# Optimization experiments

Hardware: AMD Instinct MI355X
Metric: run time of the kernel (lower is better)

Reference implementation:

```python
import jax, jax.numpy as jnp
import numpy as np

N = 50000
E = 1600000
IN_DIM = 256
HID = 64
OUT = 16
NEG_SLOPE = 0.01


def setup_inputs() -> dict:
    key = jax.random.key(0)
    ks = jax.random.split(key, 6)
    local_features = jax.random.normal(ks[0], (N, IN_DIM), dtype=jnp.float32)
    edge_index = jax.random.randint(ks[1], (2, E), 0, N, dtype=jnp.int32)
    W0 = jax.random.normal(ks[2], (IN_DIM, HID), dtype=jnp.float32) * 0.05
    a0 = jax.random.normal(ks[3], (2 * HID, 1), dtype=jnp.float32) * 0.05
    W1 = jax.random.normal(ks[4], (HID, OUT), dtype=jnp.float32) * 0.05
    a1 = jax.random.normal(ks[5], (2 * OUT, 1), dtype=jnp.float32) * 0.05
    return {"local_features": local_features, "edge_index": edge_index,
            "W0": W0, "a0": a0, "W1": W1, "a1": a1}


def _segment_softmax(scores, seg, num_segments):
    # softmax over edges sharing the same row (destination) id
    smax = jax.ops.segment_max(scores, seg, num_segments=num_segments)
    ex = jnp.exp(scores - smax[seg])
    ssum = jax.ops.segment_sum(ex, seg, num_segments=num_segments)
    return ex / ssum[seg]


def _gat_layer(H, row, col, W, a, apply_elu):
    d = W.shape[1]
    Hw = H @ W                                   # [N, d]
    # score_e = leaky_relu([Hw[row] || Hw[col]] @ a) = leaky_relu(pr[row] + pc[col])
    pr = Hw @ a[:d, 0]                           # [N]
    pc = Hw @ a[d:, 0]                           # [N]
    s = pr[row] + pc[col]                        # [E]
    s = jnp.where(s >= 0, s, NEG_SLOPE * s)      # leaky_relu
    att = _segment_softmax(s, row, Hw.shape[0])  # per-row sparse softmax (dim=1)
    # out[row] = sum_e att_e * Hw[col_e]
    out = jax.ops.segment_sum(att[:, None] * Hw[col], row, num_segments=Hw.shape[0])
    if apply_elu:
        out = jnp.where(out > 0, out, jnp.expm1(out))  # elu
    return out


def reference(local_features, edge_index, W0, a0, W1, a1):
    row = edge_index[0]
    col = edge_index[1]
    H = _gat_layer(local_features, row, col, W0, a0, apply_elu=True)
    H = _gat_layer(H, row, col, W1, a1, apply_elu=False)
    return jax.nn.log_softmax(H, axis=1)
```

## Files before the change

### kernel.cpp

```cpp
#include <hip/hip_runtime.h>
#include <hip/hip_bf16.h>
#include <math.h>

#define NN 50000
#define NE 1600000
#define BSH 9
#define BCK 98
#define BCAP 20480

typedef __attribute__((ext_vector_type(8))) short bf16x8;
typedef __attribute__((ext_vector_type(4))) float f32x4;

__device__ __forceinline__ short f2bf(float f) {
    return (short)((__float_as_uint(f) + 0x8000u) >> 16);
}
__device__ __forceinline__ float bf2f(ushort u) {
    return __uint_as_float(((unsigned)u) << 16);
}
__device__ __forceinline__ float lo16(unsigned u) { return __uint_as_float(u << 16); }
__device__ __forceinline__ float hi16(unsigned u) { return __uint_as_float(u & 0xffff0000u); }
__device__ __forceinline__ unsigned enc_f(float f) {
    unsigned u = __float_as_uint(f);
    return (u & 0x80000000u) ? ~u : (u | 0x80000000u);
}
__device__ __forceinline__ float dec_f(unsigned e) {
    return (e & 0x80000000u) ? __uint_as_float(e & 0x7FFFFFFFu)
                             : __uint_as_float(~e);
}

__global__ void initcur_kernel(int* __restrict__ gcursor, unsigned* __restrict__ maxes) {
    int b = threadIdx.x;
    if (b < BCK) gcursor[b] = b * BCAP;
    if (b < 2) maxes[b] = 0u;
}

__global__ void __launch_bounds__(1024) binA_kernel(
        const int* __restrict__ row, const int* __restrict__ col,
        int* __restrict__ gcursor, unsigned* __restrict__ staging) {
    __shared__ unsigned lds_stage[8192];
    __shared__ unsigned lds_addr[8192];
    __shared__ int lds_cnt[128];
    __shared__ int lds_off[128];
    __shared__ int wg_goff[128];
    __shared__ int wtot[2];
    int t = threadIdx.x;
    int lane = t & 63;
    int w = t >> 6;

    for (int cb = blockIdx.x * 8192; cb < NE; cb += gridDim.x * 8192) {
        int cnt_edges = NE - cb; if (cnt_edges > 8192) cnt_edges = 8192;
        if (t < 128) lds_cnt[t] = 0;
        __syncthreads();
        int myb[8]; int mylo[8]; unsigned mypk[8];
        #pragma unroll
        for (int i = 0; i < 8; ++i) {
            int idx = i * 1024 + t;
            myb[i] = -1;
            if (idx < cnt_edges) {
                int e = cb + idx;
                int r = row[e], c = col[e];
                int b = r >> BSH;
                myb[i] = b;
                mypk[i] = ((unsigned)(r & 511) << 16) | (unsigned)c;
                mylo[i] = atomicAdd(&lds_cnt[b], 1);
            }
        }
        __syncthreads();
        int v = (t < 128) ? lds_cnt[t] : 0;
        int x = v;
        #pragma unroll
        for (int off = 1; off < 64; off <<= 1) {
            int y = __shfl_up(x, off);
            if (lane >= off) x += y;
        }
        if (t < 128 && lane == 63) wtot[w] = x;
        __syncthreads();
        int add = (w == 1) ? wtot[0] : 0;
        if (t < 128) lds_off[t] = x - v + add;
        if (t < BCK) {
            int cc = lds_cnt[t];
            wg_goff[t] = cc ? atomicAdd(&gcursor[t], cc) : 0;
        }
        __syncthreads();
        #pragma unroll
        for (int i = 0; i < 8; ++i) if (myb[i] >= 0) {
            int p = lds_off[myb[i]] + mylo[i];
            lds_stage[p] = mypk[i];
            lds_addr[p] = (unsigned)(wg_goff[myb[i]] + mylo[i]);
        }
        __syncthreads();
        for (int i = t; i < cnt_edges; i += 1024)
            staging[lds_addr[i]] = lds_stage[i];
        __syncthreads();
    }
}

__global__ void bucketscan_kernel(const int* __restrict__ gcursor,
                                  int* __restrict__ bbase,
                                  int* __restrict__ rowptr) {
    __shared__ int wt0;
    int t = threadIdx.x;
    int lane = t & 63;
    int w = t >> 6;
    int v = (t < BCK) ? (gcursor[t] - t * BCAP) : 0;
    int x = v;
    #pragma unroll
    for (int off = 1; off < 64; off <<= 1) {
        int y = __shfl_up(x, off);
        if (lane >= off) x += y;
    }
    if (w == 0 && lane == 63) wt0 = x;
    __syncthreads();
    int excl = x - v + ((w == 1) ? wt0 : 0);
    if (t < BCK) bbase[t] = excl;
    if (t == BCK - 1) { bbase[BCK] = excl + v; rowptr[NN] = excl + v; }
}

__global__ void __launch_bounds__(1024) binB_kernel(
        const int* __restrict__ bbase,
        const unsigned* __restrict__ staging,
        int* __restrict__ rowptr,
        ushort* __restrict__ colperm) {
    __shared__ int cur[512];
    __shared__ int lexcl[512];
    __shared__ int wls[8];
    __shared__ ushort lds_col[BCAP];
    int b = blockIdx.x;
    int t = threadIdx.x;
    int lane = t & 63;
    int w = t >> 6;
    int rbase = b << BSH;
    int nrows = NN - rbase; if (nrows > 512) nrows = 512;
    int gbase = bbase[b];
    int cnt = bbase[b + 1] - gbase;
    if (cnt > BCAP) cnt = BCAP;
    const unsigned* sb = staging + (size_t)b * BCAP;

    if (t < 512) cur[t] = 0;
    __syncthreads();
    for (int i = t; i < cnt; i += 1024)
        atomicAdd(&cur[sb[i] >> 16], 1);
    __syncthreads();
    int v = 0, x = 0;
    if (t < 512) {
        v = cur[t];
        x = v;
        #pragma unroll
        for (int off = 1; off < 64; off <<= 1) {
            int y = __shfl_up(x, off);
            if (lane >= off) x += y;
        }
        if (lane == 63) wls[w] = x;
    }
    __syncthreads();
    if (t < 8) {
        int s = wls[t];
        #pragma unroll
        for (int off = 1; off < 8; off <<= 1) {
            int y = __shfl_up(s, off, 8);
            if ((t & 7) >= off) s += y;
        }
        wls[t] = s;
    }
    __syncthreads();
    if (t < 512) {
        int e = x - v + ((w > 0) ? wls[w - 1] : 0);
        lexcl[t] = e;
        if (t < nrows) rowptr[rbase + t] = gbase + e;
    }
    __syncthreads();
    if (t < 512) cur[t] = lexcl[t];
    __syncthreads();
    for (int i = t; i < cnt; i += 1024) {
        unsigned e = sb[i];
        int pos = atomicAdd(&cur[e >> 16], 1);
        lds_col[pos] = (ushort)(e & 0xFFFFu);
    }
    __syncthreads();
    for (int i = t; i < cnt; i += 1024)
        colperm[gbase + i] = lds_col[i];
}

__global__ void pcmax_kernel(const float* __restrict__ pc, unsigned* __restrict__ out) {
    int i = blockIdx.x * 256 + threadIdx.x;
    float v = (i < NN) ? pc[i] : -1e30f;
    #pragma unroll
    for (int off = 32; off; off >>= 1) v = fmaxf(v, __shfl_xor(v, off));
    if ((threadIdx.x & 63) == 0) atomicMax(out, enc_f(v));
}

__global__ void prep_kernel(const float* __restrict__ W, ushort* __restrict__ WTg) {
    int i = blockIdx.x * 256 + threadIdx.x;
    if (i >= 64 * 256) return;
    int n = i >> 8, k = i & 255;
    WTg[n * 264 + k] = (ushort)f2bf(W[k * 64 + n]);
}

__global__ void __launch_bounds__(256) gemm0_kernel(
        const float* __restrict__ X,
        const ushort* __restrict__ WTg,
        const float* __restrict__ a,
        __hip_bfloat16* __restrict__ Hwb,
        float* __restrict__ pr,
        float* __restrict__ pc) {
    __shared__ ushort Wt[64 * 264];
    int tid = threadIdx.x;
    {
        const uint* src = (const uint*)WTg;
        uint* dst = (uint*)Wt;
        for (int i = tid; i < 64 * 132; i += 256) dst[i] = src[i];
    }
    __syncthreads();
    int lane = tid & 63, wid = tid >> 6;
    int c = lane & 15, quad = lane >> 4;
    const ushort* wtp[4];
#pragma unroll
    for (int g = 0; g < 4; ++g) wtp[g] = &Wt[(g * 16 + c) * 264 + quad * 8];
    float aA[4], aB[4];
#pragma unroll
    for (int g = 0; g < 4; ++g) { aA[g] = a[g * 16 + c]; aB[g] = a[64 + g * 16 + c]; }

    int row0 = blockIdx.x * 128 + wid * 16;

#pragma unroll
    for (int tt = 0; tt < 2; ++tt) {
        int rt = row0 + tt * 64;
        int arow = rt + c; if (arow >= NN) arow = NN - 1;
        const float* xbase = X + (size_t)arow * 256 + quad * 8;
        f32x4 acc[4];
#pragma unroll
        for (int g = 0; g < 4; ++g) acc[g] = (f32x4){0.f, 0.f, 0.f, 0.f};

#pragma unroll
        for (int k0 = 0; k0 < 256; k0 += 32) {
            float4 xa = *(const float4*)(xbase + k0);
            float4 xb = *(const float4*)(xbase + k0 + 4);
            bf16x8 af;
            af[0] = f2bf(xa.x); af[1] = f2bf(xa.y); af[2] = f2bf(xa.z); af[3] = f2bf(xa.w);
            af[4] = f2bf(xb.x); af[5] = f2bf(xb.y); af[6] = f2bf(xb.z); af[7] = f2bf(xb.w);
#pragma unroll
            for (int g = 0; g < 4; ++g) {
                bf16x8 bg = *(const bf16x8*)(wtp[g] + k0);
                acc[g] = __builtin_amdgcn_mfma_f32_16x16x32_bf16(af, bg, acc[g], 0, 0, 0);
            }
        }

#pragma unroll
        for (int r = 0; r < 4; ++r) {
            int row = rt + quad * 4 + r;
            float v0 = acc[0][r], v1 = acc[1][r], v2 = acc[2][r], v3 = acc[3][r];
            if (row < NN) {
                __hip_bfloat16* hp = Hwb + (size_t)row * 64 + c;
                hp[0]  = __float2bfloat16(v0);
                hp[16] = __float2bfloat16(v1);
                hp[32] = __float2bfloat16(v2);
                hp[48] = __float2bfloat16(v3);
            }
            float pv = v0 * aA[0] + v1 * aA[1] + v2 * aA[2] + v3 * aA[3];
            float qv = v0 * aB[0] + v1 * aB[1] + v2 * aB[2] + v3 * aB[3];
#pragma unroll
            for (int off = 8; off; off >>= 1) {
                pv += __shfl_xor(pv, off);
                qv += __shfl_xor(qv, off);
            }
            if (c == 0 && row < NN) { pr[row] = pv; pc[row] = qv; }
        }
    }
}

__global__ void __launch_bounds__(256) node0_kernel(
        const int* __restrict__ rowptr,
        const ushort* __restrict__ colperm,
        const float* __restrict__ pr,
        const float* __restrict__ pc,
        const unsigned* __restrict__ pcmax,
        const ushort* __restrict__ Hwb,
        const float* __restrict__ W1,
        const float* __restrict__ a1,
        __hip_bfloat16* __restrict__ Hw1b,
        float* __restrict__ pr1,
        float* __restrict__ pc1) {
    __shared__ float W1s[64 * 17];
    __shared__ float a1s[32];
    __shared__ float hbuf[4][64];
    __shared__ unsigned long long wcbuf[4][64];
    int t = threadIdx.x;
    for (int i = t; i < 64 * 16; i += 256)
        W1s[(i >> 4) * 17 + (i & 15)] = W1[i];
    if (t < 32) a1s[t] = a1[t];
    __syncthreads();

    int lane = t & 63;
    int wid = t >> 6;
    int node = blockIdx.x * 4 + wid;
    int k = lane & 15, q = lane >> 4;
    int start = rowptr[node], end = rowptr[node + 1];
    float pri = pr[node];
    float m = pri + dec_f(*pcmax);
    m = (m >= 0.f) ? m : 0.01f * m;

    float wsum = 0.f;
    float acc0 = 0.f, acc1 = 0.f, acc2 = 0.f, acc3 = 0.f;
    for (int base = start; base < end; base += 64) {
        int n = end - base; if (n > 64) n = 64;
        float wv = 0.f; unsigned cv = 0;
        if (lane < n) {
            cv = (unsigned)colperm[base + lane];
            float s = pri + pc[cv];
            s = (s >= 0.f) ? s : 0.01f * s;
            wv = expf(s - m);
        }
        wsum += wv;
        wcbuf[wid][lane] = ((unsigned long long)cv << 32) |
                           (unsigned long long)__float_as_uint(wv);
        int iters = (n + 3) >> 2;
        #pragma unroll 4
        for (int jj = 0; jj < iters; ++jj) {
            unsigned long long wc = wcbuf[wid][jj * 4 + q];
            float wj = __uint_as_float((unsigned)wc);
            int cj = (int)(wc >> 32);
            ushort4 hv = *(const ushort4*)(Hwb + (size_t)cj * 64 + k * 4);
            acc0 = fmaf(wj, bf2f(hv.x), acc0);
            acc1 = fmaf(wj, bf2f(hv.y), acc1);
            acc2 = fmaf(wj, bf2f(hv.z), acc2);
            acc3 = fmaf(wj, bf2f(hv.w), acc3);
        }
    }
#pragma unroll
    for (int off = 32; off; off >>= 1) wsum += __shfl_xor(wsum, off);
    acc0 += __shfl_xor(acc0, 16); acc0 += __shfl_xor(acc0, 32);
    acc1 += __shfl_xor(acc1, 16); acc1 += __shfl_xor(acc1, 32);
    acc2 += __shfl_xor(acc2, 16); acc2 += __shfl_xor(acc2, 32);
    acc3 += __shfl_xor(acc3, 16); acc3 += __shfl_xor(acc3, 32);

    float inv = (wsum > 0.f) ? 1.f / wsum : 0.f;
    float h0 = acc0 * inv; h0 = (h0 > 0.f) ? h0 : expm1f(h0);
    float h1 = acc1 * inv; h1 = (h1 > 0.f) ? h1 : expm1f(h1);
    float h2 = acc2 * inv; h2 = (h2 > 0.f) ? h2 : expm1f(h2);
    float h3 = acc3 * inv; h3 = (h3 > 0.f) ? h3 : expm1f(h3);
    if (q == 0) {
        float4 hh = {h0, h1, h2, h3};
        *(float4*)&hbuf[wid][k * 4] = hh;
    }
    int j = lane & 15, p = lane >> 4;
    const float* hbp = hbuf[wid];
    float vj = 0.f;
#pragma unroll
    for (int i = 0; i < 16; ++i) {
        int kk = p * 16 + i;
        vj = fmaf(hbp[kk], W1s[kk * 17 + j], vj);
    }
    vj += __shfl_xor(vj, 16);
    vj += __shfl_xor(vj, 32);
    if (p == 0) Hw1b[(size_t)node * 16 + j] = __float2bfloat16(vj);
    float pv = vj * a1s[j];
    float qv = vj * a1s[16 + j];
#pragma unroll
    for (int off = 8; off; off >>= 1) {
        pv += __shfl_xor(pv, off);
        qv += __shfl_xor(qv, off);
    }
    if (lane == 0) { pr1[node] = pv; pc1[node] = qv; }
}

__global__ void __launch_bounds__(256) node1_kernel(
        const int* __restrict__ rowptr,
        const ushort* __restrict__ colperm,
        const float* __restrict__ pr,
        const float* __restrict__ pc,
        const unsigned* __restrict__ pcmax,
        const ushort* __restrict__ Hwb,
        float* __restrict__ out) {
    __shared__ unsigned long long wcbuf[4][64];
    int lane = threadIdx.x & 63;
    int wid = threadIdx.x >> 6;
    int node = blockIdx.x * 4 + wid;
    int k = lane & 7, q = lane >> 3;
    int start = rowptr[node], end = rowptr[node + 1];
    float pri = pr[node];
    float m = pri + dec_f(*pcmax);
    m = (m >= 0.f) ? m : 0.01f * m;

    float wsum = 0.f, a0 = 0.f, a1 = 0.f;
    for (int base = start; base < end; base += 64) {
        int n = end - base; if (n > 64) n = 64;
        float wv = 0.f; unsigned cv = 0;
        if (lane < n) {
            cv = (unsigned)colperm[base + lane];
            float s = pri + pc[cv];
            s = (s >= 0.f) ? s : 0.01f * s;
            wv = expf(s - m);
        }
        wsum += wv;
        wcbuf[wid][lane] = ((unsigned long long)cv << 32) |
                           (unsigned long long)__float_as_uint(wv);
        int iters = (n + 7) >> 3;
        #pragma unroll 8
        for (int jj = 0; jj < iters; ++jj) {
            unsigned long long wc = wcbuf[wid][jj * 8 + q];
            float wj = __uint_as_float((unsigned)wc);
            int cj = (int)(wc >> 32);
            unsigned hv = *(const unsigned*)(Hwb + (size_t)cj * 16 + k * 2);
            a0 = fmaf(wj, lo16(hv), a0);
            a1 = fmaf(wj, hi16(hv), a1);
        }
    }
#pragma unroll
    for (int off = 32; off; off >>= 1) wsum += __shfl_xor(wsum, off);
    a0 += __shfl_xor(a0, 8); a0 += __shfl_xor(a0, 16); a0 += __shfl_xor(a0, 32);
    a1 += __shfl_xor(a1, 8); a1 += __shfl_xor(a1, 16); a1 += __shfl_xor(a1, 32);
    float inv = (wsum > 0.f) ? 1.f / wsum : 0.f;
    float v0 = a0 * inv, v1 = a1 * inv;
    float mm = fmaxf(v0, v1);
#pragma unroll
    for (int off = 1; off < 8; off <<= 1) mm = fmaxf(mm, __shfl_xor(mm, off, 8));
    float ssx = expf(v0 - mm) + expf(v1 - mm);
#pragma unroll
    for (int off = 1; off < 8; off <<= 1) ssx += __shfl_xor(ssx, off, 8);
    float lse = mm + logf(ssx);
    if (q == 0) {
        float2 o = {v0 - lse, v1 - lse};
        *(float2*)(out + (size_t)node * 16 + k * 2) = o;
    }
}

extern "C" void kernel_launch(void* const* d_in, const int* in_sizes, int n_in,
                              void* d_out, int out_size, void* d_ws, size_t ws_size,
                              hipStream_t stream) {
    const float* X  = (const float*)d_in[0];
    const int*   ei = (const int*)d_in[1];
    const float* W0 = (const float*)d_in[2];
    const float* a0 = (const float*)d_in[3];
    const float* W1 = (const float*)d_in[4];
    const float* a1 = (const float*)d_in[5];
    float* out = (float*)d_out;

    const int* row = ei;
    const int* col = ei + NE;

    char* wsb = (char*)d_ws;
    size_t off = 0;
    auto alloc = [&](size_t bytes) {
        void* p = wsb + off;
        off += (bytes + 15) & ~(size_t)15;
        return p;
    };
    unsigned* maxes = (unsigned*)alloc(16);
    int* rowptr     = (int*)alloc((NN + 2) * 4);
    int* gcursor    = (int*)alloc(128 * 4);
    int* bbase      = (int*)alloc(128 * 4);
    unsigned* staging = (unsigned*)alloc((size_t)BCK * BCAP * 4);
    ushort* colperm = (ushort*)alloc((size_t)NE * 2);
    ushort* WTg     = (ushort*)alloc((size_t)64 * 264 * 2);
    __hip_bfloat16* Hw0b = (__hip_bfloat16*)alloc((size_t)NN * 64 * 2);
    float* pr0      = (float*)alloc(NN * 4);
    float* pc0      = (float*)alloc(NN * 4);
    __hip_bfloat16* Hw1b = (__hip_bfloat16*)alloc((size_t)NN * 16 * 2);
    float* pr1      = (float*)alloc(NN * 4);
    float* pc1      = (float*)alloc(NN * 4);

    initcur_kernel<<<1, 128, 0, stream>>>(gcursor, maxes);
    binA_kernel<<<196, 1024, 0, stream>>>(row, col, gcursor, staging);
    bucketscan_kernel<<<1, 128, 0, stream>>>(gcursor, bbase, rowptr);
    binB_kernel<<<BCK, 1024, 0, stream>>>(bbase, staging, rowptr, colperm);

    prep_kernel<<<64, 256, 0, stream>>>(W0, WTg);
    gemm0_kernel<<<(NN + 127) / 128, 256, 0, stream>>>(X, WTg, a0, Hw0b, pr0, pc0);
    pcmax_kernel<<<(NN + 255) / 256, 256, 0, stream>>>(pc0, &maxes[0]);
    node0_kernel<<<NN / 4, 256, 0, stream>>>(rowptr, colperm, pr0, pc0,
                                             &maxes[0], (const ushort*)Hw0b,
                                             W1, a1, Hw1b, pr1, pc1);

    pcmax_kernel<<<(NN + 255) / 256, 256, 0, stream>>>(pc1, &maxes[1]);
    node1_kernel<<<NN / 4, 256, 0, stream>>>(rowptr, colperm, pr1, pc1,
                                             &maxes[1], (const ushort*)Hw1b, out);
}
```

Measured before the change: 233.4 us.

## Fuse pc max into gemm0, vectorize binning loads, use packed f32x2 FMAs

The layer-0 pc max reduction now happens inside gemm0 through a per-block LDS atomicMax followed by one global atomicMax, which removes a separate pcmax kernel launch and a reread of pc0. binA now has each thread read 8 contiguous edges with int4 loads instead of strided scalar loads, and binB reads staging with uint4 loads. The gather-accumulate loops in node0 and node1 use f32x2 vector arithmetic, intended to map to packed FMA, and node0 loads Hw as uint2 with bit-shift bf16 conversion. The changed edge-to-thread mapping in binA alters the order of edges within each bucket, but the per-row order is already nondeterministic because of the atomics.

```diff
diff --git a/kernel.cpp b/kernel.cpp
--- a/kernel.cpp
+++ b/kernel.cpp
@@ -10,12 +10,10 @@
 
 typedef __attribute__((ext_vector_type(8))) short bf16x8;
 typedef __attribute__((ext_vector_type(4))) float f32x4;
+typedef __attribute__((ext_vector_type(2))) float f32x2;
 
 __device__ __forceinline__ short f2bf(float f) {
     return (short)((__float_as_uint(f) + 0x8000u) >> 16);
-}
-__device__ __forceinline__ float bf2f(ushort u) {
-    return __uint_as_float(((unsigned)u) << 16);
 }
 __device__ __forceinline__ float lo16(unsigned u) { return __uint_as_float(u << 16); }
 __device__ __forceinline__ float hi16(unsigned u) { return __uint_as_float(u & 0xffff0000u); }
@@ -52,17 +50,33 @@
         if (t < 128) lds_cnt[t] = 0;
         __syncthreads();
         int myb[8]; int mylo[8]; unsigned mypk[8];
-        #pragma unroll
-        for (int i = 0; i < 8; ++i) {
-            int idx = i * 1024 + t;
-            myb[i] = -1;
-            if (idx < cnt_edges) {
-                int e = cb + idx;
-                int r = row[e], c = col[e];
-                int b = r >> BSH;
+        int e0 = cb + t * 8;
+        if (t * 8 + 7 < cnt_edges) {
+            int4 r0 = *(const int4*)(row + e0);
+            int4 r1 = *(const int4*)(row + e0 + 4);
+            int4 c0 = *(const int4*)(col + e0);
+            int4 c1 = *(const int4*)(col + e0 + 4);
+            int rr[8] = {r0.x, r0.y, r0.z, r0.w, r1.x, r1.y, r1.z, r1.w};
+            int cc[8] = {c0.x, c0.y, c0.z, c0.w, c1.x, c1.y, c1.z, c1.w};
+            #pragma unroll
+            for (int i = 0; i < 8; ++i) {
+                int b = rr[i] >> BSH;
                 myb[i] = b;
-                mypk[i] = ((unsigned)(r & 511) << 16) | (unsigned)c;
+                mypk[i] = ((unsigned)(rr[i] & 511) << 16) | (unsigned)cc[i];
                 mylo[i] = atomicAdd(&lds_cnt[b], 1);
+            }
+        } else {
+            #pragma unroll
+            for (int i = 0; i < 8; ++i) {
+                int idx = t * 8 + i;
+                myb[i] = -1;
+                if (idx < cnt_edges) {
+                    int e = cb + idx;
+                    int r = row[e], c = col[e];
+                    myb[i] = r >> BSH;
+                    mypk[i] = ((unsigned)(r & 511) << 16) | (unsigned)c;
+                    mylo[i] = atomicAdd(&lds_cnt[myb[i]], 1);
+                }
             }
         }
         __syncthreads();
@@ -78,8 +92,8 @@
         int add = (w == 1) ? wtot[0] : 0;
         if (t < 128) lds_off[t] = x - v + add;
         if (t < BCK) {
-            int cc = lds_cnt[t];
-            wg_goff[t] = cc ? atomicAdd(&gcursor[t], cc) : 0;
+            int cc2 = lds_cnt[t];
+            wg_goff[t] = cc2 ? atomicAdd(&gcursor[t], cc2) : 0;
         }
         __syncthreads();
         #pragma unroll
@@ -135,10 +149,19 @@
     int cnt = bbase[b + 1] - gbase;
     if (cnt > BCAP) cnt = BCAP;
     const unsigned* sb = staging + (size_t)b * BCAP;
+    const uint4* sb4 = (const uint4*)sb;
+    int cnt4 = cnt >> 2;
 
     if (t < 512) cur[t] = 0;
     __syncthreads();
-    for (int i = t; i < cnt; i += 1024)
+    for (int i4 = t; i4 < cnt4; i4 += 1024) {
+        uint4 e4 = sb4[i4];
+        atomicAdd(&cur[e4.x >> 16], 1);
+        atomicAdd(&cur[e4.y >> 16], 1);
+        atomicAdd(&cur[e4.z >> 16], 1);
+        atomicAdd(&cur[e4.w >> 16], 1);
+    }
+    for (int i = cnt4 * 4 + t; i < cnt; i += 1024)
         atomicAdd(&cur[sb[i] >> 16], 1);
     __syncthreads();
     int v = 0, x = 0;
@@ -171,7 +194,14 @@
     __syncthreads();
     if (t < 512) cur[t] = lexcl[t];
     __syncthreads();
-    for (int i = t; i < cnt; i += 1024) {
+    for (int i4 = t; i4 < cnt4; i4 += 1024) {
+        uint4 e4 = sb4[i4];
+        int p0 = atomicAdd(&cur[e4.x >> 16], 1); lds_col[p0] = (ushort)(e4.x & 0xFFFFu);
+        int p1 = atomicAdd(&cur[e4.y >> 16], 1); lds_col[p1] = (ushort)(e4.y & 0xFFFFu);
+        int p2 = atomicAdd(&cur[e4.z >> 16], 1); lds_col[p2] = (ushort)(e4.z & 0xFFFFu);
+        int p3 = atomicAdd(&cur[e4.w >> 16], 1); lds_col[p3] = (ushort)(e4.w & 0xFFFFu);
+    }
+    for (int i = cnt4 * 4 + t; i < cnt; i += 1024) {
         unsigned e = sb[i];
         int pos = atomicAdd(&cur[e >> 16], 1);
         lds_col[pos] = (ushort)(e & 0xFFFFu);
@@ -202,9 +232,12 @@
         const float* __restrict__ a,
         __hip_bfloat16* __restrict__ Hwb,
         float* __restrict__ pr,
-        float* __restrict__ pc) {
+        float* __restrict__ pc,
+        unsigned* __restrict__ max0) {
     __shared__ ushort Wt[64 * 264];
+    __shared__ unsigned bmax;
     int tid = threadIdx.x;
+    if (tid == 0) bmax = 0u;
     {
         const uint* src = (const uint*)WTg;
         uint* dst = (uint*)Wt;
@@ -221,6 +254,7 @@
     for (int g = 0; g < 4; ++g) { aA[g] = a[g * 16 + c]; aB[g] = a[64 + g * 16 + c]; }
 
     int row0 = blockIdx.x * 128 + wid * 16;
+    float qmax = -1e30f;
 
 #pragma unroll
     for (int tt = 0; tt < 2; ++tt) {
@@ -264,8 +298,14 @@
                 qv += __shfl_xor(qv, off);
             }
             if (c == 0 && row < NN) { pr[row] = pv; pc[row] = qv; }
-        }
-    }
+            if (row < NN) qmax = fmaxf(qmax, qv);
+        }
+    }
+    qmax = fmaxf(qmax, __shfl_xor(qmax, 16));
+    qmax = fmaxf(qmax, __shfl_xor(qmax, 32));
+    if (lane == 0) atomicMax(&bmax, enc_f(qmax));
+    __syncthreads();
+    if (tid == 0) atomicMax(max0, bmax);
 }
 
 __global__ void __launch_bounds__(256) node0_kernel(
@@ -300,7 +340,7 @@
     m = (m >= 0.f) ? m : 0.01f * m;
 
     float wsum = 0.f;
-    float acc0 = 0.f, acc1 = 0.f, acc2 = 0.f, acc3 = 0.f;
+    f32x2 accA = {0.f, 0.f}, accB = {0.f, 0.f};
     for (int base = start; base < end; base += 64) {
         int n = end - base; if (n > 64) n = 64;
         float wv = 0.f; unsigned cv = 0;
@@ -319,15 +359,17 @@
             unsigned long long wc = wcbuf[wid][jj * 4 + q];
             float wj = __uint_as_float((unsigned)wc);
             int cj = (int)(wc >> 32);
-            ushort4 hv = *(const ushort4*)(Hwb + (size_t)cj * 64 + k * 4);
-            acc0 = fmaf(wj, bf2f(hv.x), acc0);
-            acc1 = fmaf(wj, bf2f(hv.y), acc1);
-            acc2 = fmaf(wj, bf2f(hv.z), acc2);
-            acc3 = fmaf(wj, bf2f(hv.w), acc3);
+            uint2 hv = *(const uint2*)(Hwb + (size_t)cj * 64 + k * 4);
+            f32x2 wj2 = {wj, wj};
+            f32x2 h01 = {lo16(hv.x), hi16(hv.x)};
+            f32x2 h23 = {lo16(hv.y), hi16(hv.y)};
+            accA += wj2 * h01;
+            accB += wj2 * h23;
         }
     }
 #pragma unroll
     for (int off = 32; off; off >>= 1) wsum += __shfl_xor(wsum, off);
+    float acc0 = accA.x, acc1 = accA.y, acc2 = accB.x, acc3 = accB.y;
     acc0 += __shfl_xor(acc0, 16); acc0 += __shfl_xor(acc0, 32);
     acc1 += __shfl_xor(acc1, 16); acc1 += __shfl_xor(acc1, 32);
     acc2 += __shfl_xor(acc2, 16); acc2 += __shfl_xor(acc2, 32);
@@ -381,7 +423,8 @@
     float m = pri + dec_f(*pcmax);
     m = (m >= 0.f) ? m : 0.01f * m;
 
-    float wsum = 0.f, a0 = 0.f, a1 = 0.f;
+    float wsum = 0.f;
+    f32x2 acc = {0.f, 0.f};
     for (int base = start; base < end; base += 64) {
         int n = end - base; if (n > 64) n = 64;
         float wv = 0.f; unsigned cv = 0;
@@ -401,12 +444,14 @@
             float wj = __uint_as_float((unsigned)wc);
             int cj = (int)(wc >> 32);
             unsigned hv = *(const unsigned*)(Hwb + (size_t)cj * 16 + k * 2);
-            a0 = fmaf(wj, lo16(hv), a0);
-            a1 = fmaf(wj, hi16(hv), a1);
+            f32x2 wj2 = {wj, wj};
+            f32x2 h = {lo16(hv), hi16(hv)};
+            acc += wj2 * h;
         }
     }
 #pragma unroll
     for (int off = 32; off; off >>= 1) wsum += __shfl_xor(wsum, off);
+    float a0 = acc.x, a1 = acc.y;
     a0 += __shfl_xor(a0, 8); a0 += __shfl_xor(a0, 16); a0 += __shfl_xor(a0, 32);
     a1 += __shfl_xor(a1, 8); a1 += __shfl_xor(a1, 16); a1 += __shfl_xor(a1, 32);
     float inv = (wsum > 0.f) ? 1.f / wsum : 0.f;
@@ -465,8 +510,8 @@
     binB_kernel<<<BCK, 1024, 0, stream>>>(bbase, staging, rowptr, colperm);
 
     prep_kernel<<<64, 256, 0, stream>>>(W0, WTg);
-    gemm0_kernel<<<(NN + 127) / 128, 256, 0, stream>>>(X, WTg, a0, Hw0b, pr0, pc0);
-    pcmax_kernel<<<(NN + 255) / 256, 256, 0, stream>>>(pc0, &maxes[0]);
+    gemm0_kernel<<<(NN + 127) / 128, 256, 0, stream>>>(X, WTg, a0, Hw0b, pr0, pc0,
+                                                       &maxes[0]);
     node0_kernel<<<NN / 4, 256, 0, stream>>>(rowptr, colperm, pr0, pc0,
                                              &maxes[0], (const ushort*)Hw0b,
                                              W1, a1, Hw1b, pr1, pc1);
```

Result: faster. 219.0 us (-6.2%).
